# Kernel optimization log

Measured on AMD Instinct MI355X. Metric: run time of the kernel, lower is better.

Reference implementation:

```python
import jax, jax.numpy as jnp
import numpy as np

B, D, PRE, NEXT, SC, ANT = 1000, 8, 98, 512, 32, 5  # batch, devices, split-in, split-out, subcarriers, antennas
TAU = 0.1  # noise std (tau2 in original torch.normal(0, tau2, ...))


def setup_inputs() -> dict:
    key = jax.random.key(0)
    ks = jax.random.split(key, 18)
    rn = lambda k, s, sc=0.05: (jax.random.normal(k, s, jnp.float32) * sc)
    return {
        "x": jax.random.normal(ks[0], (B, D * PRE), jnp.float32),
        "noise": jax.random.normal(ks[1], (B, SC, ANT), jnp.float32) * TAU,
        "sub_w": rn(ks[2], (D, PRE, NEXT)),
        "sub_b": rn(ks[3], (D, NEXT)),
        "ln_gamma": jnp.ones((D, NEXT), jnp.float32),
        "ln_beta": jnp.zeros((D, NEXT), jnp.float32),
        "cut_w": rn(ks[4], (D, NEXT, SC)),
        "cut_b": rn(ks[5], (D, SC)),
        "b_mat": rn(ks[6], (D, SC), 1.0),
        "h_mat": rn(ks[7], (D, SC, ANT), 1.0),
        "a_mat": rn(ks[8], (SC, ANT), 1.0),
        "cut_layer_bias": rn(ks[9], (SC,)),
        "fc3_w": rn(ks[10], (SC, 98)),
        "fc3_b": rn(ks[11], (98,)),
        "fc4_w": rn(ks[12], (98, 49)),
        "fc4_b": rn(ks[13], (49,)),
        "out_w": rn(ks[14], (49, 10)),
        "out_b": rn(ks[15], (10,)),
        "k_idx": jax.random.permutation(ks[16], SC).astype(jnp.int32),  # one-hot indicator_mat as index map
    }


def reference(x, noise, sub_w, sub_b, ln_gamma, ln_beta, cut_w, cut_b,
              b_mat, h_mat, a_mat, cut_layer_bias,
              fc3_w, fc3_b, fc4_w, fc4_b, out_w, out_b, k_idx):
    # split x into per-device chunks: torch.split along dim=1 with uniform sizes
    xs = x.reshape(B, D, PRE).transpose(1, 0, 2)                       # (D, B, PRE)
    h = jax.nn.relu(jnp.einsum('dbi,dio->dbo', xs, sub_w) + sub_b[:, None, :])
    mu = jnp.mean(h, axis=-1, keepdims=True)
    var = jnp.mean(jnp.square(h - mu), axis=-1, keepdims=True)
    h = (h - mu) * jax.lax.rsqrt(var + 1e-5) * ln_gamma[:, None, :] + ln_beta[:, None, :]
    cut = jax.nn.relu(jnp.einsum('dbo,doc->dbc', h, cut_w) + cut_b[:, None, :])  # (D, B, SC)
    # h_vec[n, j] = a_j^T h_mat[n, k(j)]  (indicator one-hot -> gather)
    h_sel = h_mat[:, k_idx, :]                                         # (D, SC, ANT)
    h_vec = jnp.einsum('dkc,kc->dk', h_sel, a_mat)                     # (D, SC)
    # received = sum_n (cut_n * b_n) * h_vec_n
    received = jnp.einsum('dbc,dc,dc->bc', cut, b_mat, h_vec)          # (B, SC)
    scaled_noise = jnp.einsum('bjc,jc->bj', noise, a_mat)              # (B, SC)
    z = jax.nn.relu(received + scaled_noise + cut_layer_bias)
    z = jax.nn.relu(z @ fc3_w + fc3_b)
    z = jax.nn.relu(z @ fc4_w + fc4_b)
    return jax.nn.log_softmax(z @ out_w + out_b, axis=1)
```

## Files before the change

### kernel.cpp

```cpp
#include <hip/hip_runtime.h>
#include <math.h>

#define B 1000
#define D 8
#define PRE 98
#define NEXT 512
#define SC 32
#define ANT 5
#define BM 32
#define NT2 32
#define KP 128

using bf16x8 = __attribute__((ext_vector_type(8))) short;
using f32x4  = __attribute__((ext_vector_type(4))) float;

static __device__ __forceinline__ unsigned short f2bf(float f) {
    union { float f; unsigned u; } v{f};
    unsigned r = (v.u + 0x7fffu + ((v.u >> 16) & 1u)) >> 16;
    return (unsigned short)r;
}
static __device__ __forceinline__ float bf2f(unsigned short h) {
    union { unsigned u; float f; } v{(unsigned)h << 16};
    return v.f;
}

__global__ __launch_bounds__(256) void k_prep(const float* __restrict__ sub_w,
                                              const float* __restrict__ cut_w,
                                              unsigned short* __restrict__ sub_wT,
                                              unsigned short* __restrict__ cut_wT) {
    __shared__ __align__(16) unsigned short tile[32][128];
    int t = threadIdx.x, bid = blockIdx.x;
    if (bid < 128) {
        int d = bid >> 4, n0 = (bid & 15) * 32;
        int nn = t & 31, kk = t >> 5;
#pragma unroll
        for (int j = 0; j < 16; ++j) {
            int k = j * 8 + kk;
            float v = (k < PRE) ? sub_w[(d * PRE + k) * NEXT + n0 + nn] : 0.f;
            tile[nn][k] = f2bf(v);
        }
        __syncthreads();
        int row = t >> 3, c0 = (t & 7) * 16;
        unsigned short* dst = sub_wT + ((size_t)(d * NEXT + n0 + row)) * KP + c0;
        *reinterpret_cast<bf16x8*>(dst)     = *reinterpret_cast<bf16x8*>(&tile[row][c0]);
        *reinterpret_cast<bf16x8*>(dst + 8) = *reinterpret_cast<bf16x8*>(&tile[row][c0 + 8]);
    } else {
        int bb = bid - 128;
        int d = bb >> 2, k0 = (bb & 3) * 128;
        int nn = t & 31, kk = t >> 5;
#pragma unroll
        for (int j = 0; j < 16; ++j) {
            int kl = j * 8 + kk;
            tile[nn][kl] = f2bf(cut_w[(d * NEXT + k0 + kl) * SC + nn]);
        }
        __syncthreads();
        int row = t >> 3, c0 = (t & 7) * 16;
        unsigned short* dst = cut_wT + ((size_t)(d * SC + row)) * NEXT + k0 + c0;
        *reinterpret_cast<bf16x8*>(dst)     = *reinterpret_cast<bf16x8*>(&tile[row][c0]);
        *reinterpret_cast<bf16x8*>(dst + 8) = *reinterpret_cast<bf16x8*>(&tile[row][c0 + 8]);
    }
}

__global__ __launch_bounds__(512) void k_main(const float* __restrict__ x,
                                              const unsigned short* __restrict__ sub_wT,
                                              const float* __restrict__ sub_b,
                                              const float* __restrict__ gamma,
                                              const float* __restrict__ beta,
                                              const unsigned short* __restrict__ cut_wT,
                                              const float* __restrict__ cut_b,
                                              const float* __restrict__ b_mat,
                                              const float* __restrict__ h_mat,
                                              const float* __restrict__ a_mat,
                                              const int* __restrict__ k_idx,
                                              float* __restrict__ part) {
    __shared__ __align__(16) unsigned short x_lds[BM][136];
    __shared__ __align__(16) unsigned short h_lds[BM][536];

    int t = threadIdx.x;
    int d = blockIdx.x >> 5;
    int tile = blockIdx.x & 31;
    int b0 = tile * BM;

    for (int idx = t; idx < BM * 136; idx += 512) {
        int r = idx / 136, i = idx - r * 136;
        int b = b0 + r;
        float v = (b < B && i < PRE) ? x[b * (D * PRE) + d * PRE + i] : 0.f;
        x_lds[r][i] = f2bf(v);
    }
    __syncthreads();

    int w = t >> 6, lane = t & 63;
    int lr = lane >> 4, lc = lane & 15;

    {
        int mt = w >> 2, nt = w & 3;
        int m0 = mt * 16, n0 = nt * 128;
        f32x4 acc[8] = {};
        const unsigned short* bw = sub_wT + (size_t)d * NEXT * KP + (size_t)(n0 + lc) * KP + lr * 8;
#pragma unroll
        for (int ks = 0; ks < 4; ++ks) {
            bf16x8 a = *reinterpret_cast<const bf16x8*>(&x_lds[m0 + lc][ks * 32 + lr * 8]);
            bf16x8 bq[8];
#pragma unroll
            for (int nf = 0; nf < 8; ++nf)
                bq[nf] = *reinterpret_cast<const bf16x8*>(bw + (size_t)nf * 16 * KP + ks * 32);
#pragma unroll
            for (int nf = 0; nf < 8; ++nf)
                acc[nf] = __builtin_amdgcn_mfma_f32_16x16x32_bf16(a, bq[nf], acc[nf], 0, 0, 0);
        }
        const float* sb = sub_b + d * NEXT;
#pragma unroll
        for (int nf = 0; nf < 8; ++nf) {
            int n = n0 + nf * 16 + lc;
            float bias = sb[n];
#pragma unroll
            for (int r = 0; r < 4; ++r) {
                int m = m0 + lr * 4 + r;
                h_lds[m][n] = f2bf(fmaxf(acc[nf][r] + bias, 0.f));
            }
        }
    }
    __syncthreads();

    {
        int row = t >> 4, l16 = t & 15;
        unsigned int* hrow = reinterpret_cast<unsigned int*>(&h_lds[row][0]);
        float s1 = 0.f, s2 = 0.f;
#pragma unroll
        for (int j = 0; j < 16; ++j) {
            unsigned int p = hrow[l16 + j * 16];
            float v0 = bf2f((unsigned short)(p & 0xffffu));
            float v1 = bf2f((unsigned short)(p >> 16));
            s1 += v0 + v1;
            s2 += v0 * v0 + v1 * v1;
        }
#pragma unroll
        for (int off = 8; off >= 1; off >>= 1) {
            s1 += __shfl_xor(s1, off, 16);
            s2 += __shfl_xor(s2, off, 16);
        }
        float mu = s1 * (1.f / NEXT);
        float var = s2 * (1.f / NEXT) - mu * mu;
        float rs = rsqrtf(var + 1e-5f);
        const float* g = gamma + d * NEXT;
        const float* be = beta + d * NEXT;
#pragma unroll
        for (int j = 0; j < 16; ++j) {
            int pi = l16 + j * 16;
            unsigned int p = hrow[pi];
            int n = pi * 2;
            float v0 = (bf2f((unsigned short)(p & 0xffffu)) - mu) * rs * g[n] + be[n];
            float v1 = (bf2f((unsigned short)(p >> 16)) - mu) * rs * g[n + 1] + be[n + 1];
            hrow[pi] = (unsigned)f2bf(v0) | ((unsigned)f2bf(v1) << 16);
        }
    }
    __syncthreads();

    if (w < 4) {
        int mt = w >> 1, nt = w & 1;
        f32x4 acc = {};
        const unsigned short* bw = cut_wT + (size_t)(d * SC + nt * 16 + lc) * NEXT + lr * 8;
#pragma unroll
        for (int ks = 0; ks < 16; ++ks) {
            bf16x8 a = *reinterpret_cast<const bf16x8*>(&h_lds[mt * 16 + lc][ks * 32 + lr * 8]);
            bf16x8 bq = *reinterpret_cast<const bf16x8*>(bw + ks * 32);
            acc = __builtin_amdgcn_mfma_f32_16x16x32_bf16(a, bq, acc, 0, 0, 0);
        }
        int c = nt * 16 + lc;
        int kk = k_idx[c];
        float hv = 0.f;
#pragma unroll
        for (int a = 0; a < ANT; ++a)
            hv = fmaf(h_mat[(d * SC + kk) * ANT + a], a_mat[c * ANT + a], hv);
        float cf = b_mat[d * SC + c] * hv;
        float cb = cut_b[d * SC + c];
#pragma unroll
        for (int r = 0; r < 4; ++r) {
            int m = mt * 16 + lr * 4 + r;
            int b = b0 + m;
            if (b < B) part[(d * B + b) * SC + c] = fmaxf(acc[r] + cb, 0.f) * cf;
        }
    }
}

__global__ __launch_bounds__(256) void k_tail(const float* __restrict__ part,
                                              const float* __restrict__ noise,
                                              const float* __restrict__ a_mat,
                                              const float* __restrict__ clb,
                                              const float* __restrict__ fc3_w,
                                              const float* __restrict__ fc3_b,
                                              const float* __restrict__ fc4_w,
                                              const float* __restrict__ fc4_b,
                                              const float* __restrict__ out_w,
                                              const float* __restrict__ out_b,
                                              float* __restrict__ out) {
    __shared__ float w3[SC * 98];
    __shared__ float w4[98 * 49];
    __shared__ float wo[49 * 10];
    __shared__ float b3[98], b4[49], bo[10];
    __shared__ float z_s[4][SC];
    __shared__ float z3_s[4][98];
    __shared__ float z4_s[4][49];

    int t = threadIdx.x;
    for (int i = t; i < SC * 98; i += 256) w3[i] = fc3_w[i];
    for (int i = t; i < 98 * 49; i += 256) w4[i] = fc4_w[i];
    for (int i = t; i < 49 * 10; i += 256) wo[i] = out_w[i];
    if (t < 98) b3[t] = fc3_b[t];
    if (t < 49) b4[t] = fc4_b[t];
    if (t < 10) bo[t] = out_b[t];
    __syncthreads();

    int w = t >> 6, lane = t & 63;
    int b = blockIdx.x * 4 + w;

    if (lane < SC) {
        int j = lane;
        float s = clb[j];
#pragma unroll
        for (int d = 0; d < D; ++d) s += part[(d * B + b) * SC + j];
#pragma unroll
        for (int a = 0; a < ANT; ++a)
            s = fmaf(noise[(b * SC + j) * ANT + a], a_mat[j * ANT + a], s);
        z_s[w][j] = fmaxf(s, 0.f);
    }
    __syncthreads();

    for (int o = lane; o < 98; o += 64) {
        float s = b3[o];
#pragma unroll
        for (int j = 0; j < SC; ++j) s = fmaf(z_s[w][j], w3[j * 98 + o], s);
        z3_s[w][o] = fmaxf(s, 0.f);
    }
    __syncthreads();

    if (lane < 49) {
        float s = b4[lane];
        for (int j = 0; j < 98; ++j) s = fmaf(z3_s[w][j], w4[j * 49 + lane], s);
        z4_s[w][lane] = fmaxf(s, 0.f);
    }
    __syncthreads();

    float v = -INFINITY;
    if (lane < 10) {
        float s = bo[lane];
        for (int j = 0; j < 49; ++j) s = fmaf(z4_s[w][j], wo[j * 10 + lane], s);
        v = s;
    }
    float m = v;
#pragma unroll
    for (int off = 8; off >= 1; off >>= 1) m = fmaxf(m, __shfl_xor(m, off, 16));
    float e = (lane < 10) ? expf(v - m) : 0.f;
    float ssum = e;
#pragma unroll
    for (int off = 8; off >= 1; off >>= 1) ssum += __shfl_xor(ssum, off, 16);
    if (lane < 10) out[b * 10 + lane] = v - m - logf(ssum);
}

extern "C" void kernel_launch(void* const* d_in, const int* in_sizes, int n_in,
                              void* d_out, int out_size, void* d_ws, size_t ws_size,
                              hipStream_t stream) {
    const float* x      = (const float*)d_in[0];
    const float* noise  = (const float*)d_in[1];
    const float* sub_w  = (const float*)d_in[2];
    const float* sub_b  = (const float*)d_in[3];
    const float* ln_g   = (const float*)d_in[4];
    const float* ln_b   = (const float*)d_in[5];
    const float* cut_w  = (const float*)d_in[6];
    const float* cut_b  = (const float*)d_in[7];
    const float* b_mat  = (const float*)d_in[8];
    const float* h_mat  = (const float*)d_in[9];
    const float* a_mat  = (const float*)d_in[10];
    const float* clb    = (const float*)d_in[11];
    const float* fc3_w  = (const float*)d_in[12];
    const float* fc3_b  = (const float*)d_in[13];
    const float* fc4_w  = (const float*)d_in[14];
    const float* fc4_b  = (const float*)d_in[15];
    const float* out_w  = (const float*)d_in[16];
    const float* out_b  = (const float*)d_in[17];
    const int*   k_idx  = (const int*)d_in[18];
    float* out = (float*)d_out;

    char* ws = (char*)d_ws;
    float* part            = (float*)ws;
    unsigned short* sub_wT = (unsigned short*)(ws + (1 << 20));
    unsigned short* cut_wT = (unsigned short*)(ws + (2 << 20));

    k_prep<<<160, 256, 0, stream>>>(sub_w, cut_w, sub_wT, cut_wT);
    k_main<<<D * NT2, 512, 0, stream>>>(x, sub_wT, sub_b, ln_g, ln_b, cut_wT,
                                        cut_b, b_mat, h_mat, a_mat, k_idx, part);
    k_tail<<<B / 4, 256, 0, stream>>>(part, noise, a_mat, clb, fc3_w, fc3_b,
                                      fc4_w, fc4_b, out_w, out_b, out);
}
```

Measured before the change: 32.79 us.

## Fuse tail MLP into main kernel via last-block atomic counter per tile

Removes the separate tail kernel. Each batch tile's last-finishing device block, found with an atomic counter plus threadfences, computes the fc3/fc4/out/log_softmax tail for that tile. Idle waves load the tail weights into LDS during the cut-layer GEMM. The first GEMM is also remapped so each wave covers both 16-row M tiles over 64 columns, which reuses the B fragments. This saves a kernel launch and the part round-trip gap, but adds a memset launch, more LDS per block that may lower occupancy, and serializes the tail onto 32 blocks.

Result: slower. 46.33 us (+41.3%).

```diff
diff --git a/kernel.cpp b/kernel.cpp
--- a/kernel.cpp
+++ b/kernel.cpp
@@ -8,8 +8,16 @@
 #define SC 32
 #define ANT 5
 #define BM 32
-#define NT2 32
+#define NTILE 32
 #define KP 128
+
+#define OW3 0
+#define OW4 3136
+#define OWO 7938
+#define OB3 8428
+#define OB4 8526
+#define OBO 8575
+#define WTOT 8585
 
 using bf16x8 = __attribute__((ext_vector_type(8))) short;
 using f32x4  = __attribute__((ext_vector_type(4))) float;
@@ -61,20 +69,35 @@
     }
 }
 
-__global__ __launch_bounds__(512) void k_main(const float* __restrict__ x,
-                                              const unsigned short* __restrict__ sub_wT,
-                                              const float* __restrict__ sub_b,
-                                              const float* __restrict__ gamma,
-                                              const float* __restrict__ beta,
-                                              const unsigned short* __restrict__ cut_wT,
-                                              const float* __restrict__ cut_b,
-                                              const float* __restrict__ b_mat,
-                                              const float* __restrict__ h_mat,
-                                              const float* __restrict__ a_mat,
-                                              const int* __restrict__ k_idx,
-                                              float* __restrict__ part) {
+__global__ __launch_bounds__(512) void k_fused(const float* __restrict__ x,
+                                               const unsigned short* __restrict__ sub_wT,
+                                               const float* __restrict__ sub_b,
+                                               const float* __restrict__ gamma,
+                                               const float* __restrict__ beta,
+                                               const unsigned short* __restrict__ cut_wT,
+                                               const float* __restrict__ cut_b,
+                                               const float* __restrict__ b_mat,
+                                               const float* __restrict__ h_mat,
+                                               const float* __restrict__ a_mat,
+                                               const int* __restrict__ k_idx,
+                                               const float* __restrict__ noise,
+                                               const float* __restrict__ clb,
+                                               const float* __restrict__ fc3_w,
+                                               const float* __restrict__ fc3_b,
+                                               const float* __restrict__ fc4_w,
+                                               const float* __restrict__ fc4_b,
+                                               const float* __restrict__ out_w,
+                                               const float* __restrict__ out_b,
+                                               float* __restrict__ part,
+                                               int* __restrict__ counters,
+                                               float* __restrict__ out) {
     __shared__ __align__(16) unsigned short x_lds[BM][136];
     __shared__ __align__(16) unsigned short h_lds[BM][536];
+    __shared__ float W_lds[WTOT];
+    __shared__ float z_s[8][SC];
+    __shared__ float z3_s[8][98];
+    __shared__ float z4_s[8][49];
+    __shared__ int last_flag;
 
     int t = threadIdx.x;
     int d = blockIdx.x >> 5;
@@ -93,31 +116,33 @@
     int lr = lane >> 4, lc = lane & 15;
 
     {
-        int mt = w >> 2, nt = w & 3;
-        int m0 = mt * 16, n0 = nt * 128;
-        f32x4 acc[8] = {};
+        int n0 = w * 64;
+        f32x4 acc[2][4] = {};
         const unsigned short* bw = sub_wT + (size_t)d * NEXT * KP + (size_t)(n0 + lc) * KP + lr * 8;
 #pragma unroll
         for (int ks = 0; ks < 4; ++ks) {
-            bf16x8 a = *reinterpret_cast<const bf16x8*>(&x_lds[m0 + lc][ks * 32 + lr * 8]);
-            bf16x8 bq[8];
-#pragma unroll
-            for (int nf = 0; nf < 8; ++nf)
+            bf16x8 a0 = *reinterpret_cast<const bf16x8*>(&x_lds[lc][ks * 32 + lr * 8]);
+            bf16x8 a1 = *reinterpret_cast<const bf16x8*>(&x_lds[16 + lc][ks * 32 + lr * 8]);
+            bf16x8 bq[4];
+#pragma unroll
+            for (int nf = 0; nf < 4; ++nf)
                 bq[nf] = *reinterpret_cast<const bf16x8*>(bw + (size_t)nf * 16 * KP + ks * 32);
 #pragma unroll
-            for (int nf = 0; nf < 8; ++nf)
-                acc[nf] = __builtin_amdgcn_mfma_f32_16x16x32_bf16(a, bq[nf], acc[nf], 0, 0, 0);
+            for (int nf = 0; nf < 4; ++nf) {
+                acc[0][nf] = __builtin_amdgcn_mfma_f32_16x16x32_bf16(a0, bq[nf], acc[0][nf], 0, 0, 0);
+                acc[1][nf] = __builtin_amdgcn_mfma_f32_16x16x32_bf16(a1, bq[nf], acc[1][nf], 0, 0, 0);
+            }
         }
         const float* sb = sub_b + d * NEXT;
 #pragma unroll
-        for (int nf = 0; nf < 8; ++nf) {
+        for (int nf = 0; nf < 4; ++nf) {
             int n = n0 + nf * 16 + lc;
             float bias = sb[n];
 #pragma unroll
-            for (int r = 0; r < 4; ++r) {
-                int m = m0 + lr * 4 + r;
-                h_lds[m][n] = f2bf(fmaxf(acc[nf][r] + bias, 0.f));
-            }
+            for (int mt = 0; mt < 2; ++mt)
+#pragma unroll
+                for (int r = 0; r < 4; ++r)
+                    h_lds[mt * 16 + lr * 4 + r][n] = f2bf(fmaxf(acc[mt][nf][r] + bias, 0.f));
         }
     }
     __syncthreads();
@@ -180,81 +205,68 @@
             int b = b0 + m;
             if (b < B) part[(d * B + b) * SC + c] = fmaxf(acc[r] + cb, 0.f) * cf;
         }
-    }
-}
-
-__global__ __launch_bounds__(256) void k_tail(const float* __restrict__ part,
-                                              const float* __restrict__ noise,
-                                              const float* __restrict__ a_mat,
-                                              const float* __restrict__ clb,
-                                              const float* __restrict__ fc3_w,
-                                              const float* __restrict__ fc3_b,
-                                              const float* __restrict__ fc4_w,
-                                              const float* __restrict__ fc4_b,
-                                              const float* __restrict__ out_w,
-                                              const float* __restrict__ out_b,
-                                              float* __restrict__ out) {
-    __shared__ float w3[SC * 98];
-    __shared__ float w4[98 * 49];
-    __shared__ float wo[49 * 10];
-    __shared__ float b3[98], b4[49], bo[10];
-    __shared__ float z_s[4][SC];
-    __shared__ float z3_s[4][98];
-    __shared__ float z4_s[4][49];
-
-    int t = threadIdx.x;
-    for (int i = t; i < SC * 98; i += 256) w3[i] = fc3_w[i];
-    for (int i = t; i < 98 * 49; i += 256) w4[i] = fc4_w[i];
-    for (int i = t; i < 49 * 10; i += 256) wo[i] = out_w[i];
-    if (t < 98) b3[t] = fc3_b[t];
-    if (t < 49) b4[t] = fc4_b[t];
-    if (t < 10) bo[t] = out_b[t];
-    __syncthreads();
-
-    int w = t >> 6, lane = t & 63;
-    int b = blockIdx.x * 4 + w;
-
-    if (lane < SC) {
-        int j = lane;
-        float s = clb[j];
-#pragma unroll
-        for (int d = 0; d < D; ++d) s += part[(d * B + b) * SC + j];
-#pragma unroll
-        for (int a = 0; a < ANT; ++a)
-            s = fmaf(noise[(b * SC + j) * ANT + a], a_mat[j * ANT + a], s);
-        z_s[w][j] = fmaxf(s, 0.f);
-    }
-    __syncthreads();
-
-    for (int o = lane; o < 98; o += 64) {
-        float s = b3[o];
-#pragma unroll
-        for (int j = 0; j < SC; ++j) s = fmaf(z_s[w][j], w3[j * 98 + o], s);
-        z3_s[w][o] = fmaxf(s, 0.f);
-    }
-    __syncthreads();
-
-    if (lane < 49) {
-        float s = b4[lane];
-        for (int j = 0; j < 98; ++j) s = fmaf(z3_s[w][j], w4[j * 49 + lane], s);
-        z4_s[w][lane] = fmaxf(s, 0.f);
-    }
-    __syncthreads();
-
-    float v = -INFINITY;
-    if (lane < 10) {
-        float s = bo[lane];
-        for (int j = 0; j < 49; ++j) s = fmaf(z4_s[w][j], wo[j * 10 + lane], s);
-        v = s;
-    }
-    float m = v;
-#pragma unroll
-    for (int off = 8; off >= 1; off >>= 1) m = fmaxf(m, __shfl_xor(m, off, 16));
-    float e = (lane < 10) ? expf(v - m) : 0.f;
-    float ssum = e;
-#pragma unroll
-    for (int off = 8; off >= 1; off >>= 1) ssum += __shfl_xor(ssum, off, 16);
-    if (lane < 10) out[b * 10 + lane] = v - m - logf(ssum);
+    } else {
+        int tt = t - 256;
+        for (int i = tt; i < 3136; i += 256) W_lds[OW3 + i] = fc3_w[i];
+        for (int i = tt; i < 4802; i += 256) W_lds[OW4 + i] = fc4_w[i];
+        for (int i = tt; i < 490; i += 256)  W_lds[OWO + i] = out_w[i];
+        if (tt < 98) W_lds[OB3 + tt] = fc3_b[tt];
+        if (tt < 49) W_lds[OB4 + tt] = fc4_b[tt];
+        if (tt < 10) W_lds[OBO + tt] = out_b[tt];
+    }
+
+    __syncthreads();
+    if (t == 0) {
+        __threadfence();
+        int old = atomicAdd(&counters[tile], 1);
+        int isl = (old == D - 1) ? 1 : 0;
+        if (isl) __threadfence();
+        last_flag = isl;
+    }
+    __syncthreads();
+    if (!last_flag) return;
+
+    for (int r = 0; r < 4; ++r) {
+        int m = w * 4 + r;
+        int b = b0 + m;
+        if (b >= B) continue;
+
+        if (lane < SC) {
+            int c = lane;
+            float s = clb[c];
+#pragma unroll
+            for (int dd = 0; dd < D; ++dd) s += part[(dd * B + b) * SC + c];
+#pragma unroll
+            for (int a = 0; a < ANT; ++a)
+                s = fmaf(noise[(b * SC + c) * ANT + a], a_mat[c * ANT + a], s);
+            z_s[w][c] = fmaxf(s, 0.f);
+        }
+        for (int o = lane; o < 98; o += 64) {
+            float s = W_lds[OB3 + o];
+#pragma unroll
+            for (int j = 0; j < SC; ++j) s = fmaf(z_s[w][j], W_lds[OW3 + j * 98 + o], s);
+            z3_s[w][o] = fmaxf(s, 0.f);
+        }
+        if (lane < 49) {
+            float s = W_lds[OB4 + lane];
+            for (int j = 0; j < 98; ++j) s = fmaf(z3_s[w][j], W_lds[OW4 + j * 49 + lane], s);
+            z4_s[w][lane] = fmaxf(s, 0.f);
+        }
+        float v = -INFINITY;
+        if (lane < 10) {
+            float s = W_lds[OBO + lane];
+            for (int j = 0; j < 49; ++j) s = fmaf(z4_s[w][j], W_lds[OWO + j * 10 + lane], s);
+            v = s;
+        }
+        float mx = v;
+#pragma unroll
+        for (int off = 8; off >= 1; off >>= 1) mx = fmaxf(mx, __shfl_xor(mx, off, 16));
+        float e = (lane < 10) ? expf(v - mx) : 0.f;
+        float ssum = e;
+#pragma unroll
+        for (int off = 8; off >= 1; off >>= 1) ssum += __shfl_xor(ssum, off, 16);
+        if (lane < 10) out[b * 10 + lane] = v - mx - logf(ssum);
+    }
 }
 
 extern "C" void kernel_launch(void* const* d_in, const int* in_sizes, int n_in,
@@ -285,10 +297,13 @@
     float* part            = (float*)ws;
     unsigned short* sub_wT = (unsigned short*)(ws + (1 << 20));
     unsigned short* cut_wT = (unsigned short*)(ws + (2 << 20));
-
+    int* counters          = (int*)(ws + (2 << 20) + (1 << 18));
+
+    hipMemsetAsync(counters, 0, NTILE * sizeof(int), stream);
     k_prep<<<160, 256, 0, stream>>>(sub_w, cut_w, sub_wT, cut_wT);
-    k_main<<<D * NT2, 512, 0, stream>>>(x, sub_wT, sub_b, ln_g, ln_b, cut_wT,
-                                        cut_b, b_mat, h_mat, a_mat, k_idx, part);
-    k_tail<<<B / 4, 256, 0, stream>>>(part, noise, a_mat, clb, fc3_w, fc3_b,
-                                      fc4_w, fc4_b, out_w, out_b, out);
-}
+    k_fused<<<D * NTILE, 512, 0, stream>>>(x, sub_wT, sub_b, ln_g, ln_b, cut_wT,
+                                           cut_b, b_mat, h_mat, a_mat, k_idx,
+                                           noise, clb, fc3_w, fc3_b, fc4_w,
+                                           fc4_b, out_w, out_b, part, counters,
+                                           out);
+}
```

## Restructure main GEMM warp tiling, split-K cut layer, transpose partials, widen tail

Applied to the files above, without the earlier changes.

In the first GEMM each warp now covers all 32 rows by 64 columns, with its weight fragments preloaded into registers, instead of 16 rows by 128 columns. The cut-layer GEMM is split across all 8 warps, two K halves each, and the halves are combined through LDS. The partial buffer layout changes from (D,B,SC) to (B,D,SC), so the tail kernel can read one batch row with a single float4 per lane and reduce across devices with shuffles. The tail kernel uses 512 threads handling 8 rows per block, stages bias and a_mat in LDS, and drops the intra-block syncs because each warp touches only its own rows. Risks are higher register pressure from the preloaded fragments and possible races, since the tail's removed syncs now depend on per-warp ordering of LDS accesses.

Result: faster. 30.24 us (-7.8%).

```diff
diff --git a/kernel.cpp b/kernel.cpp
--- a/kernel.cpp
+++ b/kernel.cpp
@@ -8,7 +8,7 @@
 #define SC 32
 #define ANT 5
 #define BM 32
-#define NT2 32
+#define NTILE 32
 #define KP 128
 
 using bf16x8 = __attribute__((ext_vector_type(8))) short;
@@ -61,20 +61,21 @@
     }
 }
 
-__global__ __launch_bounds__(512) void k_main(const float* __restrict__ x,
-                                              const unsigned short* __restrict__ sub_wT,
-                                              const float* __restrict__ sub_b,
-                                              const float* __restrict__ gamma,
-                                              const float* __restrict__ beta,
-                                              const unsigned short* __restrict__ cut_wT,
-                                              const float* __restrict__ cut_b,
-                                              const float* __restrict__ b_mat,
-                                              const float* __restrict__ h_mat,
-                                              const float* __restrict__ a_mat,
-                                              const int* __restrict__ k_idx,
-                                              float* __restrict__ part) {
+__global__ __launch_bounds__(512, 2) void k_mid(const float* __restrict__ x,
+                                                const unsigned short* __restrict__ sub_wT,
+                                                const float* __restrict__ sub_b,
+                                                const float* __restrict__ gamma,
+                                                const float* __restrict__ beta,
+                                                const unsigned short* __restrict__ cut_wT,
+                                                const float* __restrict__ cut_b,
+                                                const float* __restrict__ b_mat,
+                                                const float* __restrict__ h_mat,
+                                                const float* __restrict__ a_mat,
+                                                const int* __restrict__ k_idx,
+                                                float* __restrict__ part) {
     __shared__ __align__(16) unsigned short x_lds[BM][136];
     __shared__ __align__(16) unsigned short h_lds[BM][536];
+    __shared__ f32x4 pacc[4][64];
 
     int t = threadIdx.x;
     int d = blockIdx.x >> 5;
@@ -93,31 +94,36 @@
     int lr = lane >> 4, lc = lane & 15;
 
     {
-        int mt = w >> 2, nt = w & 3;
-        int m0 = mt * 16, n0 = nt * 128;
-        f32x4 acc[8] = {};
+        int n0 = w * 64;
         const unsigned short* bw = sub_wT + (size_t)d * NEXT * KP + (size_t)(n0 + lc) * KP + lr * 8;
+        bf16x8 bq[4][4];
+#pragma unroll
+        for (int ks = 0; ks < 4; ++ks)
+#pragma unroll
+            for (int nf = 0; nf < 4; ++nf)
+                bq[ks][nf] = *reinterpret_cast<const bf16x8*>(bw + (size_t)nf * 16 * KP + ks * 32);
+
+        f32x4 acc[2][4] = {};
 #pragma unroll
         for (int ks = 0; ks < 4; ++ks) {
-            bf16x8 a = *reinterpret_cast<const bf16x8*>(&x_lds[m0 + lc][ks * 32 + lr * 8]);
-            bf16x8 bq[8];
-#pragma unroll
-            for (int nf = 0; nf < 8; ++nf)
-                bq[nf] = *reinterpret_cast<const bf16x8*>(bw + (size_t)nf * 16 * KP + ks * 32);
-#pragma unroll
-            for (int nf = 0; nf < 8; ++nf)
-                acc[nf] = __builtin_amdgcn_mfma_f32_16x16x32_bf16(a, bq[nf], acc[nf], 0, 0, 0);
+            bf16x8 a0 = *reinterpret_cast<const bf16x8*>(&x_lds[lc][ks * 32 + lr * 8]);
+            bf16x8 a1 = *reinterpret_cast<const bf16x8*>(&x_lds[16 + lc][ks * 32 + lr * 8]);
+#pragma unroll
+            for (int nf = 0; nf < 4; ++nf) {
+                acc[0][nf] = __builtin_amdgcn_mfma_f32_16x16x32_bf16(a0, bq[ks][nf], acc[0][nf], 0, 0, 0);
+                acc[1][nf] = __builtin_amdgcn_mfma_f32_16x16x32_bf16(a1, bq[ks][nf], acc[1][nf], 0, 0, 0);
+            }
         }
         const float* sb = sub_b + d * NEXT;
 #pragma unroll
-        for (int nf = 0; nf < 8; ++nf) {
+        for (int nf = 0; nf < 4; ++nf) {
             int n = n0 + nf * 16 + lc;
             float bias = sb[n];
 #pragma unroll
-            for (int r = 0; r < 4; ++r) {
-                int m = m0 + lr * 4 + r;
-                h_lds[m][n] = f2bf(fmaxf(acc[nf][r] + bias, 0.f));
-            }
+            for (int mt = 0; mt < 2; ++mt)
+#pragma unroll
+                for (int r = 0; r < 4; ++r)
+                    h_lds[mt * 16 + lr * 4 + r][n] = f2bf(fmaxf(acc[mt][nf][r] + bias, 0.f));
         }
     }
     __syncthreads();
@@ -156,34 +162,46 @@
     }
     __syncthreads();
 
-    if (w < 4) {
-        int mt = w >> 1, nt = w & 1;
+    {
+        int kh = w >> 2, sub = w & 3;
+        int mt = sub >> 1, nt = sub & 1;
+        int kbase = kh * 256;
+        const unsigned short* bw = cut_wT + (size_t)(d * SC + nt * 16 + lc) * NEXT + kbase + lr * 8;
+        bf16x8 bq[8];
+#pragma unroll
+        for (int ks = 0; ks < 8; ++ks)
+            bq[ks] = *reinterpret_cast<const bf16x8*>(bw + ks * 32);
+
         f32x4 acc = {};
-        const unsigned short* bw = cut_wT + (size_t)(d * SC + nt * 16 + lc) * NEXT + lr * 8;
-#pragma unroll
-        for (int ks = 0; ks < 16; ++ks) {
-            bf16x8 a = *reinterpret_cast<const bf16x8*>(&h_lds[mt * 16 + lc][ks * 32 + lr * 8]);
-            bf16x8 bq = *reinterpret_cast<const bf16x8*>(bw + ks * 32);
-            acc = __builtin_amdgcn_mfma_f32_16x16x32_bf16(a, bq, acc, 0, 0, 0);
-        }
-        int c = nt * 16 + lc;
-        int kk = k_idx[c];
-        float hv = 0.f;
-#pragma unroll
-        for (int a = 0; a < ANT; ++a)
-            hv = fmaf(h_mat[(d * SC + kk) * ANT + a], a_mat[c * ANT + a], hv);
-        float cf = b_mat[d * SC + c] * hv;
-        float cb = cut_b[d * SC + c];
-#pragma unroll
-        for (int r = 0; r < 4; ++r) {
-            int m = mt * 16 + lr * 4 + r;
-            int b = b0 + m;
-            if (b < B) part[(d * B + b) * SC + c] = fmaxf(acc[r] + cb, 0.f) * cf;
-        }
-    }
-}
-
-__global__ __launch_bounds__(256) void k_tail(const float* __restrict__ part,
+#pragma unroll
+        for (int ks = 0; ks < 8; ++ks) {
+            bf16x8 a = *reinterpret_cast<const bf16x8*>(&h_lds[mt * 16 + lc][kbase + ks * 32 + lr * 8]);
+            acc = __builtin_amdgcn_mfma_f32_16x16x32_bf16(a, bq[ks], acc, 0, 0, 0);
+        }
+        if (kh == 1) pacc[sub][lane] = acc;
+        __syncthreads();
+        if (kh == 0) {
+            f32x4 o = pacc[sub][lane];
+            acc[0] += o[0]; acc[1] += o[1]; acc[2] += o[2]; acc[3] += o[3];
+            int c = nt * 16 + lc;
+            int kk = k_idx[c];
+            float hv = 0.f;
+#pragma unroll
+            for (int a = 0; a < ANT; ++a)
+                hv = fmaf(h_mat[(d * SC + kk) * ANT + a], a_mat[c * ANT + a], hv);
+            float cf = b_mat[d * SC + c] * hv;
+            float cb = cut_b[d * SC + c];
+#pragma unroll
+            for (int r = 0; r < 4; ++r) {
+                int m = mt * 16 + lr * 4 + r;
+                int b = b0 + m;
+                if (b < B) part[(b * D + d) * SC + c] = fmaxf(acc[r] + cb, 0.f) * cf;
+            }
+        }
+    }
+}
+
+__global__ __launch_bounds__(512) void k_tail(const float* __restrict__ part,
                                               const float* __restrict__ noise,
                                               const float* __restrict__ a_mat,
                                               const float* __restrict__ clb,
@@ -197,34 +215,48 @@
     __shared__ float w3[SC * 98];
     __shared__ float w4[98 * 49];
     __shared__ float wo[49 * 10];
-    __shared__ float b3[98], b4[49], bo[10];
-    __shared__ float z_s[4][SC];
-    __shared__ float z3_s[4][98];
-    __shared__ float z4_s[4][49];
+    __shared__ float b3[98], b4[49], bo[10], clb_s[SC], am_s[SC * ANT];
+    __shared__ float z_s[8][SC];
+    __shared__ float z3_s[8][98];
+    __shared__ float z4_s[8][49];
 
     int t = threadIdx.x;
-    for (int i = t; i < SC * 98; i += 256) w3[i] = fc3_w[i];
-    for (int i = t; i < 98 * 49; i += 256) w4[i] = fc4_w[i];
-    for (int i = t; i < 49 * 10; i += 256) wo[i] = out_w[i];
+    for (int i = t; i < SC * 98; i += 512) w3[i] = fc3_w[i];
+    for (int i = t; i < 98 * 49; i += 512) w4[i] = fc4_w[i];
+    for (int i = t; i < 49 * 10; i += 512) wo[i] = out_w[i];
     if (t < 98) b3[t] = fc3_b[t];
     if (t < 49) b4[t] = fc4_b[t];
     if (t < 10) bo[t] = out_b[t];
+    if (t >= 128 && t < 128 + SC) clb_s[t - 128] = clb[t - 128];
+    if (t >= 192 && t < 192 + SC * ANT) am_s[t - 192] = a_mat[t - 192];
     __syncthreads();
 
     int w = t >> 6, lane = t & 63;
-    int b = blockIdx.x * 4 + w;
-
-    if (lane < SC) {
-        int j = lane;
-        float s = clb[j];
-#pragma unroll
-        for (int d = 0; d < D; ++d) s += part[(d * B + b) * SC + j];
-#pragma unroll
-        for (int a = 0; a < ANT; ++a)
-            s = fmaf(noise[(b * SC + j) * ANT + a], a_mat[j * ANT + a], s);
-        z_s[w][j] = fmaxf(s, 0.f);
-    }
-    __syncthreads();
+    int b = blockIdx.x * 8 + w;
+
+    {
+        float4 v = *reinterpret_cast<const float4*>(part + (size_t)b * (D * SC) + lane * 4);
+#pragma unroll
+        for (int off = 8; off <= 32; off <<= 1) {
+            v.x += __shfl_xor(v.x, off);
+            v.y += __shfl_xor(v.y, off);
+            v.z += __shfl_xor(v.z, off);
+            v.w += __shfl_xor(v.w, off);
+        }
+        if (lane < 8) {
+            int cc = lane * 4;
+            float s[4] = {v.x, v.y, v.z, v.w};
+#pragma unroll
+            for (int i = 0; i < 4; ++i) {
+                int c = cc + i;
+                float zz = s[i] + clb_s[c];
+#pragma unroll
+                for (int a = 0; a < ANT; ++a)
+                    zz = fmaf(noise[(b * SC + c) * ANT + a], am_s[c * ANT + a], zz);
+                z_s[w][c] = fmaxf(zz, 0.f);
+            }
+        }
+    }
 
     for (int o = lane; o < 98; o += 64) {
         float s = b3[o];
@@ -232,29 +264,25 @@
         for (int j = 0; j < SC; ++j) s = fmaf(z_s[w][j], w3[j * 98 + o], s);
         z3_s[w][o] = fmaxf(s, 0.f);
     }
-    __syncthreads();
-
     if (lane < 49) {
         float s = b4[lane];
         for (int j = 0; j < 98; ++j) s = fmaf(z3_s[w][j], w4[j * 49 + lane], s);
         z4_s[w][lane] = fmaxf(s, 0.f);
     }
-    __syncthreads();
-
     float v = -INFINITY;
     if (lane < 10) {
         float s = bo[lane];
         for (int j = 0; j < 49; ++j) s = fmaf(z4_s[w][j], wo[j * 10 + lane], s);
         v = s;
     }
-    float m = v;
-#pragma unroll
-    for (int off = 8; off >= 1; off >>= 1) m = fmaxf(m, __shfl_xor(m, off, 16));
-    float e = (lane < 10) ? expf(v - m) : 0.f;
+    float mx = v;
+#pragma unroll
+    for (int off = 8; off >= 1; off >>= 1) mx = fmaxf(mx, __shfl_xor(mx, off, 16));
+    float e = (lane < 10) ? expf(v - mx) : 0.f;
     float ssum = e;
 #pragma unroll
     for (int off = 8; off >= 1; off >>= 1) ssum += __shfl_xor(ssum, off, 16);
-    if (lane < 10) out[b * 10 + lane] = v - m - logf(ssum);
+    if (lane < 10) out[b * 10 + lane] = v - mx - logf(ssum);
 }
 
 extern "C" void kernel_launch(void* const* d_in, const int* in_sizes, int n_in,
@@ -287,8 +315,8 @@
     unsigned short* cut_wT = (unsigned short*)(ws + (2 << 20));
 
     k_prep<<<160, 256, 0, stream>>>(sub_w, cut_w, sub_wT, cut_wT);
-    k_main<<<D * NT2, 512, 0, stream>>>(x, sub_wT, sub_b, ln_g, ln_b, cut_wT,
-                                        cut_b, b_mat, h_mat, a_mat, k_idx, part);
-    k_tail<<<B / 4, 256, 0, stream>>>(part, noise, a_mat, clb, fc3_w, fc3_b,
-                                      fc4_w, fc4_b, out_w, out_b, out);
-}
+    k_mid<<<D * NTILE, 512, 0, stream>>>(x, sub_wT, sub_b, ln_g, ln_b, cut_wT,
+                                         cut_b, b_mat, h_mat, a_mat, k_idx, part);
+    k_tail<<<125, 512, 0, stream>>>(part, noise, a_mat, clb, fc3_w, fc3_b,
+                                    fc4_w, fc4_b, out_w, out_b, out);
+}
```
